# Kernel optimization log

Hardware: AMD Instinct MI355X
Metric: run time of the kernel (lower is better)

## Reference

```python
import jax, jax.numpy as jnp
import numpy as np

WAYS, SHOTS = 5, 5
F_DIM, HID = 1024, 512          # num_node_feats, int(1024*0.5)
BATCH = 2048                    # num_tasks
N = WAYS * SHOTS + 1            # 26 samples per episode
BN_EPS = 1e-5


def setup_inputs() -> dict:
    key = jax.random.key(0)
    ks = jax.random.split(key, 12)
    d = {"node_feats": jax.random.normal(ks[0], (BATCH, N, F_DIM), jnp.float32)}
    # conv1 (1x1): F_DIM -> HID, bn1; conv2: HID -> HID, bn2; conv4: HID -> F_DIM
    d["w1"] = jax.random.normal(ks[1], (HID, F_DIM), jnp.float32) * (1.0 / np.sqrt(F_DIM))
    d["b1"] = jax.random.normal(ks[2], (HID,), jnp.float32) * 0.01
    d["g1"] = jnp.ones((HID,), jnp.float32)
    d["be1"] = jnp.zeros((HID,), jnp.float32)
    d["m1"] = jax.random.normal(ks[3], (HID,), jnp.float32) * 0.1
    d["v1"] = jax.random.uniform(ks[4], (HID,), jnp.float32, 0.5, 1.5)
    d["w2"] = jax.random.normal(ks[5], (HID, HID), jnp.float32) * (1.0 / np.sqrt(HID))
    d["b2"] = jax.random.normal(ks[6], (HID,), jnp.float32) * 0.01
    d["g2"] = jnp.ones((HID,), jnp.float32)
    d["be2"] = jnp.zeros((HID,), jnp.float32)
    d["m2"] = jax.random.normal(ks[7], (HID,), jnp.float32) * 0.1
    d["v2"] = jax.random.uniform(ks[8], (HID,), jnp.float32, 0.5, 1.5)
    d["w3"] = jax.random.normal(ks[9], (F_DIM, HID), jnp.float32) * (1.0 / np.sqrt(HID))
    d["b3"] = jax.random.normal(ks[10], (F_DIM,), jnp.float32) * 0.01
    return d


def _conv1x1(x, w, b):
    # x: [B, Cin, N], w: [Cout, Cin] -> [B, Cout, N]
    return jnp.einsum('bcn,oc->bon', x, w) + b[None, :, None]


def _bn(x, g, be, m, v):
    # inference BatchNorm1d over channel dim of [B, C, N]
    scale = g / jnp.sqrt(v + BN_EPS)
    return (x - m[None, :, None]) * scale[None, :, None] + be[None, :, None]


def _forward(node_feats, w1, b1, g1, be1, m1, v1, w2, b2, g2, be2, m2, v2, w3, b3):
    B, n, F = node_feats.shape  # n == WAYS*SHOTS+1
    # in-place per-class mean on the transpose view also mutates node_feats in torch:
    sup = node_feats[:, :WAYS * SHOTS].reshape(B, WAYS, SHOTS, F)
    sup = jnp.broadcast_to(sup.mean(axis=2, keepdims=True), sup.shape).reshape(B, WAYS * SHOTS, F)
    nf = jnp.concatenate([sup, node_feats[:, WAYS * SHOTS:]], axis=1)  # [B, N, F]

    x = nf.transpose(0, 2, 1)  # [B, F, N]
    x = jax.nn.leaky_relu(_bn(_conv1x1(x, w1, b1), g1, be1, m1, v1), 0.01)
    x = jax.nn.leaky_relu(_bn(_conv1x1(x, w2, b2), g2, be2, m2, v2), 0.01)
    att = jax.nn.sigmoid(_conv1x1(x, w3, b3))  # [B, F, N]

    # sim_cal: cosine sim of u_ij = a_i*a_j*x_i vs v_ij = a_i*a_j*x_j, fused into matmuls.
    a = att.transpose(0, 2, 1)       # [B, N, F]
    a2 = a * a                       # attention squared
    P = a2 * nf                      # dot(u,v)   = (P P^T)[i,j]
    Q = a2 * nf * nf                 # ||u_ij||^2 = (Q a2^T)[i,j]
    dots = jnp.einsum('bif,bjf->bij', P, P)    # [B, N, N]
    n2 = jnp.einsum('bif,bjf->bij', Q, a2)     # [B, N, N]
    nrm = jnp.sqrt(n2)
    sim = dots / (nrm * nrm.transpose(0, 2, 1))
    pred = jnp.stack([sim, 1.0 - sim], axis=1)  # [B, 2, N, N]
    return jnp.clip(pred, 0.0, 1.0)


def reference(node_feats, w1, b1, g1, be1, m1, v1, w2, b2, g2, be2, m2, v2, w3, b3):
    return _forward(node_feats, w1, b1, g1, be1, m1, v1, w2, b2, g2, be2, m2, v2, w3, b3)
```

## Files before the change

### kernel.cpp

```cpp
#include <hip/hip_runtime.h>
#include <hip/hip_bf16.h>
#include <math.h>

typedef __bf16 bf16_t;
typedef bf16_t bf16x8 __attribute__((ext_vector_type(8)));
typedef bf16_t bf16x4 __attribute__((ext_vector_type(4)));
typedef float f32x4 __attribute__((ext_vector_type(4)));

#define WAYS 5
#define SHOTS 5
#define F_DIM 1024
#define HID 512
#define BATCH 2048
#define NN 26
#define NC 6
#define MROWS (BATCH * NC)

#define S1 (HID * F_DIM)
#define S2 (HID * HID)
#define S3 (F_DIM * HID)
#define CVT_BLOCKS ((S1 + S2 + S3) / 512)

__global__ __launch_bounds__(128)
void prep_kernel(const float* __restrict__ node,
                 const float* __restrict__ w1, const float* __restrict__ w2,
                 const float* __restrict__ w3, bf16_t* __restrict__ wall,
                 bf16_t* __restrict__ nfc_b) {
    if (blockIdx.x < CVT_BLOCKS) {
        int i = (blockIdx.x * 128 + threadIdx.x) * 4;
        const float* src;
        int j = i;
        if (i < S1)            { src = w1; }
        else if (i < S1 + S2)  { src = w2; j = i - S1; }
        else                   { src = w3; j = i - S1 - S2; }
        float4 v = *(const float4*)(src + j);
        bf16x4 o;
        o[0] = (bf16_t)v.x; o[1] = (bf16_t)v.y; o[2] = (bf16_t)v.z; o[3] = (bf16_t)v.w;
        *(bf16x4*)(wall + i) = o;
        return;
    }
    int row = blockIdx.x - CVT_BLOCKS;
    int b = row / NC;
    int w = row - b * NC;
    int f = threadIdx.x * 8;
    const float* src = node + (size_t)b * NN * F_DIM;
    float acc[8];
    if (w < WAYS) {
        #pragma unroll
        for (int e = 0; e < 8; ++e) acc[e] = 0.f;
        #pragma unroll
        for (int s = 0; s < SHOTS; ++s) {
            const float* r = src + (size_t)(w * SHOTS + s) * F_DIM + f;
            float4 v0 = *(const float4*)r;
            float4 v1 = *(const float4*)(r + 4);
            acc[0] += v0.x; acc[1] += v0.y; acc[2] += v0.z; acc[3] += v0.w;
            acc[4] += v1.x; acc[5] += v1.y; acc[6] += v1.z; acc[7] += v1.w;
        }
        #pragma unroll
        for (int e = 0; e < 8; ++e) acc[e] *= 0.2f;
    } else {
        const float* r = src + (size_t)25 * F_DIM + f;
        float4 v0 = *(const float4*)r;
        float4 v1 = *(const float4*)(r + 4);
        acc[0] = v0.x; acc[1] = v0.y; acc[2] = v0.z; acc[3] = v0.w;
        acc[4] = v1.x; acc[5] = v1.y; acc[6] = v1.z; acc[7] = v1.w;
    }
    bf16x8 ob;
    #pragma unroll
    for (int e = 0; e < 8; ++e) ob[e] = (bf16_t)acc[e];
    *(bf16x8*)(nfc_b + (size_t)row * F_DIM + f) = ob;
}

template<int EPI, int TN>
__global__ __launch_bounds__(256)
void gemm_bt(const bf16_t* __restrict__ A, const bf16_t* __restrict__ W,
             bf16_t* __restrict__ C, int M, int N, int K,
             const float* __restrict__ bias, const float* __restrict__ gam,
             const float* __restrict__ bet, const float* __restrict__ mu,
             const float* __restrict__ var) {
    constexpr int NI = TN / 32;
    __shared__ bf16_t As[2][128 * 32];
    __shared__ bf16_t Bs[2][TN * 32];
    const int tid = threadIdx.x;
    const int lane = tid & 63, wid = tid >> 6;

    const int nwg = gridDim.x * gridDim.y;
    const int orig = blockIdx.y * gridDim.x + blockIdx.x;
    const int wg = (orig & 7) * (nwg >> 3) + (orig >> 3);
    const int bxi = wg & (gridDim.x - 1);
    const int byi = wg / gridDim.x;
    const int bm = byi * 128, bn = bxi * TN;

    const int l15 = lane & 15, quad = lane >> 4;
    const int wm = (wid & 1) * 64, wn = (wid >> 1) * (TN / 2);

    const int srowA = wid * 32;
    const int srowB = wid * (TN / 4);
    const int lrow = lane >> 2;
    const int lcol = (lane & 3) * 8;
    const bf16_t* gA = A + (size_t)(bm + srowA + lrow) * K + lcol;
    const bf16_t* gB = W + (size_t)(bn + srowB + lrow) * K + lcol;

    f32x4 acc[4][NI] = {};

    auto stage = [&](int buf, int k0) {
        bf16_t* lA = &As[buf][srowA * 32];
        bf16_t* lB = &Bs[buf][srowB * 32];
        #pragma unroll
        for (int q = 0; q < 2; ++q)
            __builtin_amdgcn_global_load_lds(
                (const __attribute__((address_space(1))) void*)(gA + (size_t)q * 16 * K + k0),
                (__attribute__((address_space(3))) void*)(lA + q * 16 * 32), 16, 0, 0);
        #pragma unroll
        for (int q = 0; q < TN / 64; ++q)
            __builtin_amdgcn_global_load_lds(
                (const __attribute__((address_space(1))) void*)(gB + (size_t)q * 16 * K + k0),
                (__attribute__((address_space(3))) void*)(lB + q * 16 * 32), 16, 0, 0);
    };

    stage(0, 0);
    __syncthreads();
    int cur = 0;
    for (int k0 = 0; k0 < K; k0 += 32) {
        if (k0 + 32 < K) stage(cur ^ 1, k0 + 32);
        bf16x8 af[4], bfr[NI];
        #pragma unroll
        for (int mi = 0; mi < 4; ++mi)
            af[mi] = *(const bf16x8*)&As[cur][(wm + mi * 16 + l15) * 32 + quad * 8];
        #pragma unroll
        for (int ni = 0; ni < NI; ++ni)
            bfr[ni] = *(const bf16x8*)&Bs[cur][(wn + ni * 16 + l15) * 32 + quad * 8];
        #pragma unroll
        for (int mi = 0; mi < 4; ++mi)
            #pragma unroll
            for (int ni = 0; ni < NI; ++ni)
                acc[mi][ni] = __builtin_amdgcn_mfma_f32_16x16x32_bf16(af[mi], bfr[ni], acc[mi][ni], 0, 0, 0);
        __syncthreads();
        cur ^= 1;
    }

    #pragma unroll
    for (int ni = 0; ni < NI; ++ni) {
        const int n = bn + wn + ni * 16 + l15;
        float s, t;
        if constexpr (EPI == 0) {
            float sg = gam[n] * rsqrtf(var[n] + 1e-5f);
            s = sg;
            t = (bias[n] - mu[n]) * sg + bet[n];
        } else {
            s = 1.0f;
            t = bias[n];
        }
        #pragma unroll
        for (int mi = 0; mi < 4; ++mi) {
            const int m = bm + wm + mi * 16 + quad * 4;
            #pragma unroll
            for (int r = 0; r < 4; ++r) {
                float y = acc[mi][ni][r] * s + t;
                if constexpr (EPI == 0) {
                    y = y > 0.0f ? y : 0.01f * y;
                } else {
                    y = 1.0f / (1.0f + __expf(-y));
                }
                C[(size_t)(m + r) * N + n] = (bf16_t)y;
            }
        }
    }
}

__global__ __launch_bounds__(256)
void sim_kernel(const bf16_t* __restrict__ nfc, const bf16_t* __restrict__ att,
                float* __restrict__ out) {
    __shared__ float dmat[NC * NC], n2mat[NC * NC], simc[NC * NC];
    const int b = blockIdx.x, tid = threadIdx.x;
    const bf16_t* xs = nfc + (size_t)b * NC * F_DIM;
    const bf16_t* as = att + (size_t)b * NC * F_DIM;
    const int lane = tid & 63, wid = tid >> 6;
    for (int t = wid; t < 21; t += 4) {
        const int i = (t >= 6) + (t >= 11) + (t >= 15) + (t >= 18) + (t >= 20);
        const int j = t - (i * (13 - i)) / 2 + i;
        float d = 0.f, qij = 0.f, qji = 0.f;
        #pragma unroll
        for (int c = 0; c < 2; ++c) {
            const int f0 = lane * 8 + c * 512;
            bf16x8 vai = *(const bf16x8*)&as[i * F_DIM + f0];
            bf16x8 vaj = *(const bf16x8*)&as[j * F_DIM + f0];
            bf16x8 vxi = *(const bf16x8*)&xs[i * F_DIM + f0];
            bf16x8 vxj = *(const bf16x8*)&xs[j * F_DIM + f0];
            #pragma unroll
            for (int e = 0; e < 8; ++e) {
                float ai = (float)vai[e], aj = (float)vaj[e];
                float xi = (float)vxi[e], xj = (float)vxj[e];
                float a2i = ai * ai, a2j = aj * aj;
                float pi = a2i * xi, pj = a2j * xj;
                d   += pi * pj;
                qij += pi * xi * a2j;
                qji += pj * xj * a2i;
            }
        }
        #pragma unroll
        for (int off = 32; off > 0; off >>= 1) {
            d   += __shfl_xor(d, off);
            qij += __shfl_xor(qij, off);
            qji += __shfl_xor(qji, off);
        }
        if (lane == 0) {
            dmat[i * NC + j] = d; dmat[j * NC + i] = d;
            n2mat[i * NC + j] = qij; n2mat[j * NC + i] = qji;
        }
    }
    __syncthreads();
    if (tid < NC * NC) {
        int i = tid / NC, j = tid - (tid / NC) * NC;
        simc[tid] = dmat[tid] * rsqrtf(n2mat[i * NC + j] * n2mat[j * NC + i]);
    }
    __syncthreads();
    float* o = out + (size_t)b * (2 * NN * NN);
    for (int g = tid; g < 2 * NN * NN / 4; g += 256) {
        const int e = g * 4;
        const int ch = e / (NN * NN);
        float4 v;
        float* pv = &v.x;
        #pragma unroll
        for (int u = 0; u < 4; ++u) {
            int rem = e + u - ch * (NN * NN);
            int i = rem / NN, j = rem - (rem / NN) * NN;
            float s = simc[(i / 5) * NC + (j / 5)];
            float w = ch ? 1.0f - s : s;
            pv[u] = fminf(fmaxf(w, 0.0f), 1.0f);
        }
        *(float4*)(o + e) = v;
    }
}

extern "C" void kernel_launch(void* const* d_in, const int* in_sizes, int n_in,
                              void* d_out, int out_size, void* d_ws, size_t ws_size,
                              hipStream_t stream) {
    const float* node = (const float*)d_in[0];
    const float* w1  = (const float*)d_in[1];
    const float* b1  = (const float*)d_in[2];
    const float* g1  = (const float*)d_in[3];
    const float* be1 = (const float*)d_in[4];
    const float* m1  = (const float*)d_in[5];
    const float* v1  = (const float*)d_in[6];
    const float* w2  = (const float*)d_in[7];
    const float* b2  = (const float*)d_in[8];
    const float* g2  = (const float*)d_in[9];
    const float* be2 = (const float*)d_in[10];
    const float* m2  = (const float*)d_in[11];
    const float* v2  = (const float*)d_in[12];
    const float* w3  = (const float*)d_in[13];
    const float* b3  = (const float*)d_in[14];
    float* out = (float*)d_out;

    char* ws = (char*)d_ws;
    size_t off = 0;
    bf16_t* wall  = (bf16_t*)(ws + off); off += (size_t)(S1 + S2 + S3) * 2;
    bf16_t* w1b = wall, *w2b = wall + S1, *w3b = wall + S1 + S2;
    bf16_t* nfc_b = (bf16_t*)(ws + off); off += (size_t)MROWS * F_DIM * 2;
    bf16_t* x1    = (bf16_t*)(ws + off); off += (size_t)MROWS * HID * 2;
    bf16_t* x2    = (bf16_t*)(ws + off); off += (size_t)MROWS * HID * 2;
    bf16_t* attb  = (bf16_t*)(ws + off); off += (size_t)MROWS * F_DIM * 2;

    prep_kernel<<<CVT_BLOCKS + MROWS, 128, 0, stream>>>(node, w1, w2, w3, wall, nfc_b);
    gemm_bt<0, 128><<<dim3(HID / 128, MROWS / 128), 256, 0, stream>>>(
        nfc_b, w1b, x1, MROWS, HID, F_DIM, b1, g1, be1, m1, v1);
    gemm_bt<0, 128><<<dim3(HID / 128, MROWS / 128), 256, 0, stream>>>(
        x1, w2b, x2, MROWS, HID, HID, b2, g2, be2, m2, v2);
    gemm_bt<1, 128><<<dim3(F_DIM / 128, MROWS / 128), 256, 0, stream>>>(
        x2, w3b, attb, MROWS, F_DIM, HID, b3, nullptr, nullptr, nullptr, nullptr);
    sim_kernel<<<BATCH, 256, 0, stream>>>(nfc_b, attb, out);
}
```

Before: 410.1 us.

## Triple-buffer GEMM LDS staging with vmcnt waits; use 64-wide tiles for HID GEMMs

Moves the GEMM main loop from double to triple buffering in LDS. Loads for tile k+2 are issued before computing tile k, and each iteration waits with a partial s_waitcnt vmcnt plus a raw barrier instead of a full __syncthreads, so global loads overlap more with MFMA. The first two GEMMs also switch to TN=64, which doubles their workgroup count for better CU occupancy. The cost is more LDS per block and hand-counted vmcnt values that depend on how many loads each stage issues.

```diff
diff --git a/kernel.cpp b/kernel.cpp
--- a/kernel.cpp
+++ b/kernel.cpp
@@ -79,8 +79,9 @@
              const float* __restrict__ bet, const float* __restrict__ mu,
              const float* __restrict__ var) {
     constexpr int NI = TN / 32;
-    __shared__ bf16_t As[2][128 * 32];
-    __shared__ bf16_t Bs[2][TN * 32];
+    constexpr int LPS = 2 + TN / 64;
+    __shared__ bf16_t As[3][128 * 32];
+    __shared__ bf16_t Bs[3][TN * 32];
     const int tid = threadIdx.x;
     const int lane = tid & 63, wid = tid >> 6;
 
@@ -119,24 +120,42 @@
     };
 
     stage(0, 0);
-    __syncthreads();
-    int cur = 0;
+    stage(1, 32);
+    if constexpr (TN == 64) asm volatile("s_waitcnt vmcnt(3)" ::: "memory");
+    else                    asm volatile("s_waitcnt vmcnt(4)" ::: "memory");
+    __builtin_amdgcn_s_barrier();
+    __builtin_amdgcn_sched_barrier(0);
+
+    int bufc = 0;
     for (int k0 = 0; k0 < K; k0 += 32) {
-        if (k0 + 32 < K) stage(cur ^ 1, k0 + 32);
+        const bool more2 = (k0 + 64 < K);
+        if (more2) {
+            int b2 = bufc + 2; if (b2 >= 3) b2 -= 3;
+            stage(b2, k0 + 64);
+        }
         bf16x8 af[4], bfr[NI];
         #pragma unroll
         for (int mi = 0; mi < 4; ++mi)
-            af[mi] = *(const bf16x8*)&As[cur][(wm + mi * 16 + l15) * 32 + quad * 8];
+            af[mi] = *(const bf16x8*)&As[bufc][(wm + mi * 16 + l15) * 32 + quad * 8];
         #pragma unroll
         for (int ni = 0; ni < NI; ++ni)
-            bfr[ni] = *(const bf16x8*)&Bs[cur][(wn + ni * 16 + l15) * 32 + quad * 8];
+            bfr[ni] = *(const bf16x8*)&Bs[bufc][(wn + ni * 16 + l15) * 32 + quad * 8];
         #pragma unroll
         for (int mi = 0; mi < 4; ++mi)
             #pragma unroll
             for (int ni = 0; ni < NI; ++ni)
                 acc[mi][ni] = __builtin_amdgcn_mfma_f32_16x16x32_bf16(af[mi], bfr[ni], acc[mi][ni], 0, 0, 0);
-        __syncthreads();
-        cur ^= 1;
+        if (k0 + 32 < K) {
+            if (more2) {
+                if constexpr (TN == 64) asm volatile("s_waitcnt vmcnt(3)" ::: "memory");
+                else                    asm volatile("s_waitcnt vmcnt(4)" ::: "memory");
+            } else {
+                asm volatile("s_waitcnt vmcnt(0)" ::: "memory");
+            }
+            __builtin_amdgcn_s_barrier();
+            __builtin_amdgcn_sched_barrier(0);
+        }
+        ++bufc; if (bufc == 3) bufc = 0;
     }
 
     #pragma unroll
@@ -263,9 +282,9 @@
     bf16_t* attb  = (bf16_t*)(ws + off); off += (size_t)MROWS * F_DIM * 2;
 
     prep_kernel<<<CVT_BLOCKS + MROWS, 128, 0, stream>>>(node, w1, w2, w3, wall, nfc_b);
-    gemm_bt<0, 128><<<dim3(HID / 128, MROWS / 128), 256, 0, stream>>>(
+    gemm_bt<0, 64><<<dim3(HID / 64, MROWS / 128), 256, 0, stream>>>(
         nfc_b, w1b, x1, MROWS, HID, F_DIM, b1, g1, be1, m1, v1);
-    gemm_bt<0, 128><<<dim3(HID / 128, MROWS / 128), 256, 0, stream>>>(
+    gemm_bt<0, 64><<<dim3(HID / 64, MROWS / 128), 256, 0, stream>>>(
         x1, w2b, x2, MROWS, HID, HID, b2, g2, be2, m2, v2);
     gemm_bt<1, 128><<<dim3(F_DIM / 128, MROWS / 128), 256, 0, stream>>>(
         x2, w3b, attb, MROWS, F_DIM, HID, b3, nullptr, nullptr, nullptr, nullptr);
```

New measurement: 425.6 us. 1.04x slower.

## Fuse third GEMM with sigmoid and similarity partials, shrink GEMM N-tile

Applied to the files above, without the earlier changes.

The third 1x1 conv GEMM now writes its sigmoid attention tile to shared memory and immediately computes per-episode similarity partial sums against the matching node-feature slice. This avoids writing and re-reading the full bf16 attention tensor. A small finish kernel reduces the 8 column-block partials and writes the output. The first two GEMMs also drop to a 64-wide N tile, which doubles their block count. The cost is an extra kernel launch and a partials buffer, and the smaller tiles give the first two GEMMs less data reuse per block.

```diff
diff --git a/kernel.cpp b/kernel.cpp
--- a/kernel.cpp
+++ b/kernel.cpp
@@ -20,6 +20,8 @@
 #define S2 (HID * HID)
 #define S3 (F_DIM * HID)
 #define CVT_BLOCKS ((S1 + S2 + S3) / 512)
+
+#define AP 136
 
 __global__ __launch_bounds__(128)
 void prep_kernel(const float* __restrict__ node,
@@ -71,13 +73,13 @@
     *(bf16x8*)(nfc_b + (size_t)row * F_DIM + f) = ob;
 }
 
-template<int EPI, int TN>
 __global__ __launch_bounds__(256)
 void gemm_bt(const bf16_t* __restrict__ A, const bf16_t* __restrict__ W,
              bf16_t* __restrict__ C, int M, int N, int K,
              const float* __restrict__ bias, const float* __restrict__ gam,
              const float* __restrict__ bet, const float* __restrict__ mu,
              const float* __restrict__ var) {
+    constexpr int TN = 64;
     constexpr int NI = TN / 32;
     __shared__ bf16_t As[2][128 * 32];
     __shared__ bf16_t Bs[2][TN * 32];
@@ -111,11 +113,9 @@
             __builtin_amdgcn_global_load_lds(
                 (const __attribute__((address_space(1))) void*)(gA + (size_t)q * 16 * K + k0),
                 (__attribute__((address_space(3))) void*)(lA + q * 16 * 32), 16, 0, 0);
-        #pragma unroll
-        for (int q = 0; q < TN / 64; ++q)
-            __builtin_amdgcn_global_load_lds(
-                (const __attribute__((address_space(1))) void*)(gB + (size_t)q * 16 * K + k0),
-                (__attribute__((address_space(3))) void*)(lB + q * 16 * 32), 16, 0, 0);
+        __builtin_amdgcn_global_load_lds(
+            (const __attribute__((address_space(1))) void*)(gB + k0),
+            (__attribute__((address_space(3))) void*)lB, 16, 0, 0);
     };
 
     stage(0, 0);
@@ -142,26 +142,16 @@
     #pragma unroll
     for (int ni = 0; ni < NI; ++ni) {
         const int n = bn + wn + ni * 16 + l15;
-        float s, t;
-        if constexpr (EPI == 0) {
-            float sg = gam[n] * rsqrtf(var[n] + 1e-5f);
-            s = sg;
-            t = (bias[n] - mu[n]) * sg + bet[n];
-        } else {
-            s = 1.0f;
-            t = bias[n];
-        }
+        float sg = gam[n] * rsqrtf(var[n] + 1e-5f);
+        float s = sg;
+        float t = (bias[n] - mu[n]) * sg + bet[n];
         #pragma unroll
         for (int mi = 0; mi < 4; ++mi) {
             const int m = bm + wm + mi * 16 + quad * 4;
             #pragma unroll
             for (int r = 0; r < 4; ++r) {
                 float y = acc[mi][ni][r] * s + t;
-                if constexpr (EPI == 0) {
-                    y = y > 0.0f ? y : 0.01f * y;
-                } else {
-                    y = 1.0f / (1.0f + __expf(-y));
-                }
+                y = y > 0.0f ? y : 0.01f * y;
                 C[(size_t)(m + r) * N + n] = (bf16_t)y;
             }
         }
@@ -169,54 +159,144 @@
 }
 
 __global__ __launch_bounds__(256)
-void sim_kernel(const bf16_t* __restrict__ nfc, const bf16_t* __restrict__ att,
-                float* __restrict__ out) {
-    __shared__ float dmat[NC * NC], n2mat[NC * NC], simc[NC * NC];
-    const int b = blockIdx.x, tid = threadIdx.x;
-    const bf16_t* xs = nfc + (size_t)b * NC * F_DIM;
-    const bf16_t* as = att + (size_t)b * NC * F_DIM;
+void gemm3_sim(const bf16_t* __restrict__ A, const bf16_t* __restrict__ W,
+               const float* __restrict__ bias, const bf16_t* __restrict__ nfc,
+               float* __restrict__ part) {
+    constexpr int K = HID;
+    __shared__ __align__(16) char smem[2 * (96 + 128) * 32 * 2];
+    bf16_t* As = (bf16_t*)smem;
+    bf16_t* Bs = (bf16_t*)(smem + 2 * 96 * 32 * 2);
+    bf16_t* att_s = (bf16_t*)smem;
+
+    const int tid = threadIdx.x;
     const int lane = tid & 63, wid = tid >> 6;
-    for (int t = wid; t < 21; t += 4) {
-        const int i = (t >= 6) + (t >= 11) + (t >= 15) + (t >= 18) + (t >= 20);
-        const int j = t - (i * (13 - i)) / 2 + i;
+
+    const int nwg = gridDim.x * gridDim.y;
+    const int orig = blockIdx.y * gridDim.x + blockIdx.x;
+    const int wg = (orig & 7) * (nwg >> 3) + (orig >> 3);
+    const int bxi = wg & 7;
+    const int byi = wg >> 3;
+    const int bm = byi * 96, bn = bxi * 128;
+
+    const int l15 = lane & 15, quad = lane >> 4;
+    const int wm = (wid & 1) * 48, wn = (wid >> 1) * 64;
+
+    const int lrow = lane >> 2;
+    const int lcol = (lane & 3) * 8;
+
+    f32x4 acc[3][4] = {};
+
+    auto stage = [&](int buf, int k0) {
+        for (int c = wid; c < 14; c += 4) {
+            if (c < 6) {
+                const bf16_t* g = A + (size_t)(bm + c * 16 + lrow) * K + lcol + k0;
+                bf16_t* l = As + buf * (96 * 32) + c * 16 * 32;
+                __builtin_amdgcn_global_load_lds(
+                    (const __attribute__((address_space(1))) void*)g,
+                    (__attribute__((address_space(3))) void*)l, 16, 0, 0);
+            } else {
+                const int cc = c - 6;
+                const bf16_t* g = W + (size_t)(bn + cc * 16 + lrow) * K + lcol + k0;
+                bf16_t* l = Bs + buf * (128 * 32) + cc * 16 * 32;
+                __builtin_amdgcn_global_load_lds(
+                    (const __attribute__((address_space(1))) void*)g,
+                    (__attribute__((address_space(3))) void*)l, 16, 0, 0);
+            }
+        }
+    };
+
+    stage(0, 0);
+    __syncthreads();
+    int cur = 0;
+    for (int k0 = 0; k0 < K; k0 += 32) {
+        if (k0 + 32 < K) stage(cur ^ 1, k0 + 32);
+        bf16x8 af[3], bfr[4];
+        #pragma unroll
+        for (int mi = 0; mi < 3; ++mi)
+            af[mi] = *(const bf16x8*)&As[cur * (96 * 32) + (wm + mi * 16 + l15) * 32 + quad * 8];
+        #pragma unroll
+        for (int ni = 0; ni < 4; ++ni)
+            bfr[ni] = *(const bf16x8*)&Bs[cur * (128 * 32) + (wn + ni * 16 + l15) * 32 + quad * 8];
+        #pragma unroll
+        for (int mi = 0; mi < 3; ++mi)
+            #pragma unroll
+            for (int ni = 0; ni < 4; ++ni)
+                acc[mi][ni] = __builtin_amdgcn_mfma_f32_16x16x32_bf16(af[mi], bfr[ni], acc[mi][ni], 0, 0, 0);
+        __syncthreads();
+        cur ^= 1;
+    }
+
+    #pragma unroll
+    for (int ni = 0; ni < 4; ++ni) {
+        const int nl = wn + ni * 16 + l15;
+        const float t = bias[bn + nl];
+        #pragma unroll
+        for (int mi = 0; mi < 3; ++mi) {
+            const int ml = wm + mi * 16 + quad * 4;
+            #pragma unroll
+            for (int r = 0; r < 4; ++r) {
+                float y = acc[mi][ni][r] + t;
+                y = 1.0f / (1.0f + __expf(-y));
+                att_s[(ml + r) * AP + nl] = (bf16_t)y;
+            }
+        }
+    }
+    __syncthreads();
+
+    const int sg = tid >> 4;
+    const int sl = tid & 15;
+    for (int task = sg; task < 16 * 21; task += 16) {
+        const int ep = task / 21, pr = task - ep * 21;
+        const int i = (pr >= 6) + (pr >= 11) + (pr >= 15) + (pr >= 18) + (pr >= 20);
+        const int j = pr - (i * (13 - i)) / 2 + i;
+        const int ri = ep * 6 + i, rj = ep * 6 + j;
+        bf16x8 va_i = *(const bf16x8*)&att_s[ri * AP + sl * 8];
+        bf16x8 va_j = *(const bf16x8*)&att_s[rj * AP + sl * 8];
+        bf16x8 vx_i = *(const bf16x8*)&nfc[(size_t)(bm + ri) * F_DIM + bn + sl * 8];
+        bf16x8 vx_j = *(const bf16x8*)&nfc[(size_t)(bm + rj) * F_DIM + bn + sl * 8];
         float d = 0.f, qij = 0.f, qji = 0.f;
         #pragma unroll
-        for (int c = 0; c < 2; ++c) {
-            const int f0 = lane * 8 + c * 512;
-            bf16x8 vai = *(const bf16x8*)&as[i * F_DIM + f0];
-            bf16x8 vaj = *(const bf16x8*)&as[j * F_DIM + f0];
-            bf16x8 vxi = *(const bf16x8*)&xs[i * F_DIM + f0];
-            bf16x8 vxj = *(const bf16x8*)&xs[j * F_DIM + f0];
-            #pragma unroll
-            for (int e = 0; e < 8; ++e) {
-                float ai = (float)vai[e], aj = (float)vaj[e];
-                float xi = (float)vxi[e], xj = (float)vxj[e];
-                float a2i = ai * ai, a2j = aj * aj;
-                float pi = a2i * xi, pj = a2j * xj;
-                d   += pi * pj;
-                qij += pi * xi * a2j;
-                qji += pj * xj * a2i;
-            }
-        }
-        #pragma unroll
-        for (int off = 32; off > 0; off >>= 1) {
+        for (int e = 0; e < 8; ++e) {
+            float ai = (float)va_i[e], aj = (float)va_j[e];
+            float xi = (float)vx_i[e], xj = (float)vx_j[e];
+            float a2i = ai * ai, a2j = aj * aj;
+            float pi = a2i * xi, pj = a2j * xj;
+            d   += pi * pj;
+            qij += pi * xi * a2j;
+            qji += pj * xj * a2i;
+        }
+        #pragma unroll
+        for (int off = 1; off < 16; off <<= 1) {
             d   += __shfl_xor(d, off);
             qij += __shfl_xor(qij, off);
             qji += __shfl_xor(qji, off);
         }
-        if (lane == 0) {
-            dmat[i * NC + j] = d; dmat[j * NC + i] = d;
-            n2mat[i * NC + j] = qij; n2mat[j * NC + i] = qji;
-        }
-    }
-    __syncthreads();
-    if (tid < NC * NC) {
-        int i = tid / NC, j = tid - (tid / NC) * NC;
-        simc[tid] = dmat[tid] * rsqrtf(n2mat[i * NC + j] * n2mat[j * NC + i]);
+        if (sl == 0) {
+            float* p = part + (((size_t)(byi * 16 + ep) * 8 + bxi) * 21 + pr) * 3;
+            p[0] = d; p[1] = qij; p[2] = qji;
+        }
+    }
+}
+
+__global__ __launch_bounds__(128)
+void finish_kernel(const float* __restrict__ part, float* __restrict__ out) {
+    __shared__ float simc[NC * NC];
+    const int b = blockIdx.x, tid = threadIdx.x;
+    if (tid < 21) {
+        float d = 0.f, qij = 0.f, qji = 0.f;
+        #pragma unroll
+        for (int x = 0; x < 8; ++x) {
+            const float* q = part + (((size_t)b * 8 + x) * 21 + tid) * 3;
+            d += q[0]; qij += q[1]; qji += q[2];
+        }
+        const int i = (tid >= 6) + (tid >= 11) + (tid >= 15) + (tid >= 18) + (tid >= 20);
+        const int j = tid - (i * (13 - i)) / 2 + i;
+        const float s = d * rsqrtf(qij * qji);
+        simc[i * NC + j] = s; simc[j * NC + i] = s;
     }
     __syncthreads();
     float* o = out + (size_t)b * (2 * NN * NN);
-    for (int g = tid; g < 2 * NN * NN / 4; g += 256) {
+    for (int g = tid; g < 2 * NN * NN / 4; g += 128) {
         const int e = g * 4;
         const int ch = e / (NN * NN);
         float4 v;
@@ -260,14 +340,13 @@
     bf16_t* nfc_b = (bf16_t*)(ws + off); off += (size_t)MROWS * F_DIM * 2;
     bf16_t* x1    = (bf16_t*)(ws + off); off += (size_t)MROWS * HID * 2;
     bf16_t* x2    = (bf16_t*)(ws + off); off += (size_t)MROWS * HID * 2;
-    bf16_t* attb  = (bf16_t*)(ws + off); off += (size_t)MROWS * F_DIM * 2;
+    float*  part  = (float*)(ws + off);  off += (size_t)BATCH * 8 * 21 * 3 * 4;
 
     prep_kernel<<<CVT_BLOCKS + MROWS, 128, 0, stream>>>(node, w1, w2, w3, wall, nfc_b);
-    gemm_bt<0, 128><<<dim3(HID / 128, MROWS / 128), 256, 0, stream>>>(
+    gemm_bt<<<dim3(HID / 64, MROWS / 128), 256, 0, stream>>>(
         nfc_b, w1b, x1, MROWS, HID, F_DIM, b1, g1, be1, m1, v1);
-    gemm_bt<0, 128><<<dim3(HID / 128, MROWS / 128), 256, 0, stream>>>(
+    gemm_bt<<<dim3(HID / 64, MROWS / 128), 256, 0, stream>>>(
         x1, w2b, x2, MROWS, HID, HID, b2, g2, be2, m2, v2);
-    gemm_bt<1, 128><<<dim3(F_DIM / 128, MROWS / 128), 256, 0, stream>>>(
-        x2, w3b, attb, MROWS, F_DIM, HID, b3, nullptr, nullptr, nullptr, nullptr);
-    sim_kernel<<<BATCH, 256, 0, stream>>>(nfc_b, attb, out);
-}
+    gemm3_sim<<<dim3(8, MROWS / 96), 256, 0, stream>>>(x2, w3b, b3, nfc_b, part);
+    finish_kernel<<<BATCH, 128, 0, stream>>>(part, out);
+}
```

Measured after the change: 429.8 us. 4.8% more time.
